# Kernel optimization log

Measured on AMD Instinct MI355X. Metric: run time of the kernel, lower is better.

## Reference

```python
import math
import jax, jax.numpy as jnp
import numpy as np

B, T, C, H = 4, 2048, 1024, 16
D = C // H  # head dim = 64


def setup_inputs() -> dict:
    key = jax.random.key(0)
    ks = jax.random.split(key, 5)
    s = 0.02  # trunc_normal-like init scale
    return {
        "x":  jax.random.normal(ks[0], (B, T, C), dtype=jnp.float32),
        "wq": jax.random.normal(ks[1], (C, C), dtype=jnp.float32) * s,
        "bq": jnp.zeros((C,), dtype=jnp.float32),
        "wk": jax.random.normal(ks[2], (C, C), dtype=jnp.float32) * s,
        "bk": jnp.zeros((C,), dtype=jnp.float32),
        "wv": jax.random.normal(ks[3], (C, C), dtype=jnp.float32) * s,
        "bv": jnp.zeros((C,), dtype=jnp.float32),
        "wp": jax.random.normal(ks[4], (C, C), dtype=jnp.float32) * s,
        "bp": jnp.zeros((C,), dtype=jnp.float32),
    }


def reference(x, wq, bq, wk, bk, wv, bv, wp, bp):
    b, t, c = x.shape
    # QKV projections -> (B, H, T, D)
    q = (x @ wq + bq).reshape(b, t, H, D).transpose(0, 2, 1, 3)
    k = (x @ wk + bk).reshape(b, t, H, D).transpose(0, 2, 1, 3)
    v = (x @ wv + bv).reshape(b, t, H, D).transpose(0, 2, 1, 3)
    present = jnp.stack((k, v))  # (2, B, H, T, D)
    # scaled dot-product with causal mask (layer_past is None path)
    att = jnp.einsum('bhqd,bhkd->bhqk', q, k) * (1.0 / math.sqrt(D))
    causal = jnp.tril(jnp.ones((t, t), dtype=bool))  # (T, T)
    att = jnp.where(causal[None, None], att, -jnp.inf)
    att = jax.nn.softmax(att, axis=-1)
    # dropout prob = 0.0 (eval) -> identity
    y = jnp.einsum('bhqk,bhkd->bhqd', att, v)
    y = y.transpose(0, 2, 1, 3).reshape(b, t, c)
    y = y @ wp + bp
    return (y, present)
```

## Files before the change

kernel.cpp:

```cpp
#include <hip/hip_runtime.h>
#include <hip/hip_bf16.h>
#include <stdint.h>

typedef unsigned short u16;
typedef __bf16 bf16x8 __attribute__((ext_vector_type(8)));
typedef __bf16 bf16x4 __attribute__((ext_vector_type(4)));
typedef float f32x4 __attribute__((ext_vector_type(4)));

#define BB 4
#define TT 2048
#define CC 1024
#define HH 16
#define DD 64

#define QSCALE 0.18033688011112042f

__device__ __forceinline__ u16 f2bf(float f) {
  union { float f; unsigned int u; } v; v.f = f;
  unsigned int u = v.u;
  unsigned int r = (u + 0x7fffu + ((u >> 16) & 1u)) >> 16;
  return (u16)r;
}

__device__ __forceinline__ void async_copy16(const void* g, void* l) {
  __builtin_amdgcn_global_load_lds(
      (const __attribute__((address_space(1))) void*)g,
      (__attribute__((address_space(3))) void*)l, 16, 0, 0);
}

__global__ __launch_bounds__(256) void k_cast_x(const float* __restrict__ x,
                                                u16* __restrict__ xb) {
  int i = (blockIdx.x * 256 + threadIdx.x) * 4;
  float4 f = *reinterpret_cast<const float4*>(x + i);
  ushort4 o;
  o.x = f2bf(f.x); o.y = f2bf(f.y); o.z = f2bf(f.z); o.w = f2bf(f.w);
  *reinterpret_cast<ushort4*>(xb + i) = o;
}

__global__ __launch_bounds__(256) void k_transpose_w(
    const float* __restrict__ w0, const float* __restrict__ w1,
    const float* __restrict__ w2, const float* __restrict__ w3,
    u16* __restrict__ t0, u16* __restrict__ t1,
    u16* __restrict__ t2, u16* __restrict__ t3) {
  const float* w = blockIdx.z == 0 ? w0 : blockIdx.z == 1 ? w1 : blockIdx.z == 2 ? w2 : w3;
  u16* t = blockIdx.z == 0 ? t0 : blockIdx.z == 1 ? t1 : blockIdx.z == 2 ? t2 : t3;
  __shared__ u16 tile[32][33];
  int tx = threadIdx.x, ty = threadIdx.y;
  int k0 = blockIdx.x * 32, n0 = blockIdx.y * 32;
#pragma unroll
  for (int r = 0; r < 4; r++)
    tile[ty + r * 8][tx] = f2bf(w[(size_t)(k0 + ty + r * 8) * CC + n0 + tx]);
  __syncthreads();
#pragma unroll
  for (int r = 0; r < 4; r++)
    t[(size_t)(n0 + ty + r * 8) * CC + k0 + tx] = tile[tx][ty + r * 8];
}

__global__ __launch_bounds__(256) void k_transpose_v(
    const float* __restrict__ out_v, u16* __restrict__ vbt) {
  int tb = blockIdx.x * 64;
  int bh = blockIdx.y;
  const float* src = out_v + (size_t)bh * TT * DD;
  u16* dst = vbt + (size_t)bh * TT * DD;
  __shared__ u16 tile[64][65];
  int tid = threadIdx.x;
#pragma unroll
  for (int p = 0; p < 4; p++) {
    int c = p * 256 + tid;
    int t = c >> 4, d0 = (c & 15) * 4;
    float4 f = *reinterpret_cast<const float4*>(src + (size_t)(tb + t) * DD + d0);
    tile[t][d0 + 0] = f2bf(f.x);
    tile[t][d0 + 1] = f2bf(f.y);
    tile[t][d0 + 2] = f2bf(f.z);
    tile[t][d0 + 3] = f2bf(f.w);
  }
  __syncthreads();
#pragma unroll
  for (int p = 0; p < 2; p++) {
    int c = p * 256 + tid;
    int d = c >> 3, t0 = (c & 7) * 8;
    ushort4 lo, hi;
    lo.x = tile[t0 + 0][d]; lo.y = tile[t0 + 1][d];
    lo.z = tile[t0 + 2][d]; lo.w = tile[t0 + 3][d];
    hi.x = tile[t0 + 4][d]; hi.y = tile[t0 + 5][d];
    hi.z = tile[t0 + 6][d]; hi.w = tile[t0 + 7][d];
    u16* o = dst + (size_t)d * TT + tb + t0;
    *reinterpret_cast<ushort4*>(o) = lo;
    *reinterpret_cast<ushort4*>(o + 4) = hi;
  }
}

#define GEMM_PROLOGUE()                                                        \
  int tid = threadIdx.x;                                                       \
  int lane = tid & 63;                                                         \
  int wave = tid >> 6;                                                         \
  int l15 = lane & 15, quad = lane >> 4;                                       \
  int wave_m = wave & 1, wave_n = wave >> 1;                                   \
  __shared__ u16 lA[128 * 32];                                                 \
  __shared__ u16 lB[128 * 32];                                                 \
  f32x4 acc[4][4] = {};                                                        \
  for (int k0 = 0; k0 < CC; k0 += 32) {                                        \
    __syncthreads();                                                           \
    _Pragma("unroll")                                                          \
    for (int r = 0; r < 2; r++) {                                              \
      int c = r * 256 + tid;                                                   \
      int row = c >> 2, col8 = (c & 3) * 8;                                    \
      async_copy16(A + (size_t)(tile_m + row) * CC + k0 + col8, &lA[c * 8]);   \
    }                                                                          \
    _Pragma("unroll")                                                          \
    for (int r = 0; r < 2; r++) {                                              \
      int c = r * 256 + tid;                                                   \
      int row = c >> 2, col8 = (c & 3) * 8;                                    \
      async_copy16(Bt + (size_t)(tile_n + row) * CC + k0 + col8, &lB[c * 8]);  \
    }                                                                          \
    __syncthreads();                                                           \
    bf16x8 af[4], bfr[4];                                                      \
    _Pragma("unroll")                                                          \
    for (int i = 0; i < 4; i++)                                                \
      af[i] = *reinterpret_cast<const bf16x8*>(                                \
          &lA[(wave_m * 64 + i * 16 + l15) * 32 + quad * 8]);                  \
    _Pragma("unroll")                                                          \
    for (int j = 0; j < 4; j++)                                                \
      bfr[j] = *reinterpret_cast<const bf16x8*>(                               \
          &lB[(wave_n * 64 + j * 16 + l15) * 32 + quad * 8]);                  \
    _Pragma("unroll")                                                          \
    for (int i = 0; i < 4; i++)                                                \
      _Pragma("unroll")                                                        \
      for (int j = 0; j < 4; j++)                                              \
        acc[i][j] =                                                            \
            __builtin_amdgcn_mfma_f32_16x16x32_bf16(af[i], bfr[j], acc[i][j],  \
                                                    0, 0, 0);                  \
  }

__global__ __launch_bounds__(256) void k_gemm_qkv(
    const u16* __restrict__ xb,
    const u16* __restrict__ wtq, const u16* __restrict__ wtk, const u16* __restrict__ wtv,
    const float* __restrict__ bq, const float* __restrict__ bk, const float* __restrict__ bv,
    u16* __restrict__ qb, u16* __restrict__ kb,
    float* __restrict__ out_k, float* __restrict__ out_v) {
  int mat = blockIdx.z;
  const u16* A = xb;
  const u16* Bt = mat == 0 ? wtq : mat == 1 ? wtk : wtv;
  const float* bias = mat == 0 ? bq : mat == 1 ? bk : bv;
  int tile_m = blockIdx.x * 128;
  int tile_n = blockIdx.y * 128;

  GEMM_PROLOGUE()

#pragma unroll
  for (int j = 0; j < 4; j++) {
    int n = tile_n + wave_n * 64 + j * 16 + l15;
    int h = n >> 6, d = n & 63;
    float bias_n = bias[n];
#pragma unroll
    for (int i = 0; i < 4; i++) {
#pragma unroll
      for (int r = 0; r < 4; r++) {
        int m = tile_m + wave_m * 64 + i * 16 + quad * 4 + r;
        int b = m >> 11, t = m & 2047;
        float val = acc[i][j][r] + bias_n;
        size_t idx = (((size_t)(b * HH + h)) * TT + t) * DD + d;
        if (mat == 0) {
          qb[idx] = f2bf(val * QSCALE);
        } else if (mat == 1) {
          out_k[idx] = val;
          kb[idx] = f2bf(val);
        } else {
          out_v[idx] = val;
        }
      }
    }
  }
}

__global__ __launch_bounds__(256) void k_gemm_proj(
    const u16* __restrict__ yb, const u16* __restrict__ wtp,
    const float* __restrict__ bp, float* __restrict__ out) {
  const u16* A = yb;
  const u16* Bt = wtp;
  int tile_m = blockIdx.x * 128;
  int tile_n = blockIdx.y * 128;

  GEMM_PROLOGUE()

#pragma unroll
  for (int j = 0; j < 4; j++) {
    int n = tile_n + wave_n * 64 + j * 16 + l15;
    float bias_n = bp[n];
#pragma unroll
    for (int i = 0; i < 4; i++) {
#pragma unroll
      for (int r = 0; r < 4; r++) {
        int m = tile_m + wave_m * 64 + i * 16 + quad * 4 + r;
        out[(size_t)m * CC + n] = acc[i][j][r] + bias_n;
      }
    }
  }
}

__global__ __launch_bounds__(256) void k_attn(
    const u16* __restrict__ qb, const u16* __restrict__ kbuf,
    const u16* __restrict__ vtb, u16* __restrict__ yatt) {
  int qpair = blockIdx.x;
  int bh = blockIdx.y;
  int tid = threadIdx.x;
  int lane = tid & 63;
  int wave = tid >> 6;
  int l15 = lane & 15, quad = lane >> 4;

  const u16* Q = qb + (size_t)bh * TT * DD;
  const u16* K = kbuf + (size_t)bh * TT * DD;
  const u16* Vt = vtb + (size_t)bh * TT * DD;

  __shared__ u16 kl[2][64 * 64];
  __shared__ u16 vl[2][64 * 64];
  __shared__ u16 pl[4][16 * 64];
  u16* plw = pl[wave];

  int h = bh & 15, b = bh >> 4;

  int c0 = tid, c1 = tid + 256;
  int r0 = c0 >> 3, e0 = (((c0 & 7) * 16) ^ ((r0 & 7) << 4)) >> 1;
  int r1 = c1 >> 3, e1 = (((c1 & 7) * 16) ^ ((r1 & 7) << 4)) >> 1;

  auto stage = [&](int buf, int kb0) {
    async_copy16(K + (size_t)(kb0 + r0) * DD + e0, &kl[buf][c0 * 8]);
    async_copy16(K + (size_t)(kb0 + r1) * DD + e1, &kl[buf][c1 * 8]);
    async_copy16(Vt + (size_t)r0 * TT + kb0 + e0, &vl[buf][c0 * 8]);
    async_copy16(Vt + (size_t)r1 * TT + kb0 + e1, &vl[buf][c1 * 8]);
  };

  u16* prow = plw + l15 * 64;
  int xrp = (l15 & 7) << 4;
  int q8 = quad << 3;

#pragma unroll
  for (int side = 0; side < 2; side++) {
    int qt = side == 0 ? qpair : 31 - qpair;

    int qr = qt * 64 + wave * 16 + l15;
    bf16x8 qf0 = *reinterpret_cast<const bf16x8*>(Q + (size_t)qr * DD + quad * 8);
    bf16x8 qf1 = *reinterpret_cast<const bf16x8*>(Q + (size_t)qr * DD + 32 + quad * 8);

    f32x4 o_acc[4] = {};
    float m_run = -1e30f, l_run = 0.f;

    stage(0, 0);

    for (int kblk = 0; kblk <= qt; kblk++) {
      int cur = kblk & 1;
      if (kblk < qt) {
        stage(cur ^ 1, (kblk + 1) * 64);
        asm volatile("s_waitcnt vmcnt(4)" ::: "memory");
      } else {
        asm volatile("s_waitcnt vmcnt(0)" ::: "memory");
      }
      __builtin_amdgcn_sched_barrier(0);
      __builtin_amdgcn_s_barrier();
      __builtin_amdgcn_sched_barrier(0);

      f32x4 s_acc[4];
      __builtin_amdgcn_s_setprio(1);
#pragma unroll
      for (int nb = 0; nb < 4; nb++) {
        int krow = nb * 16 + l15;
        int xr = (krow & 7) << 4;
        const u16* kp = &kl[cur][krow * 64];
        bf16x8 kf0 = *reinterpret_cast<const bf16x8*>(kp + (((quad * 16) ^ xr) >> 1));
        bf16x8 kf1 = *reinterpret_cast<const bf16x8*>(kp + (((64 + quad * 16) ^ xr) >> 1));
        f32x4 z = {};
        z = __builtin_amdgcn_mfma_f32_16x16x32_bf16(kf0, qf0, z, 0, 0, 0);
        z = __builtin_amdgcn_mfma_f32_16x16x32_bf16(kf1, qf1, z, 0, 0, 0);
        s_acc[nb] = z;
      }
      __builtin_amdgcn_s_setprio(0);

      float mx = -1e30f;
      if (kblk == qt) {
        int qg = wave * 16 + l15;
#pragma unroll
        for (int nb = 0; nb < 4; nb++)
#pragma unroll
          for (int r = 0; r < 4; r++) {
            int kg = nb * 16 + quad * 4 + r;
            float s = s_acc[nb][r];
            s = (kg <= qg) ? s : -1e30f;
            s_acc[nb][r] = s;
            mx = fmaxf(mx, s);
          }
      } else {
#pragma unroll
        for (int nb = 0; nb < 4; nb++)
#pragma unroll
          for (int r = 0; r < 4; r++) mx = fmaxf(mx, s_acc[nb][r]);
      }
      mx = fmaxf(mx, __shfl_xor(mx, 16, 64));
      mx = fmaxf(mx, __shfl_xor(mx, 32, 64));

      if (!__all(mx - m_run <= 8.0f)) {
        float mnew = fmaxf(m_run, mx);
        float alpha = __builtin_amdgcn_exp2f(m_run - mnew);
        m_run = mnew;
        l_run *= alpha;
        float av[4];
#pragma unroll
        for (int r = 0; r < 4; r++) av[r] = __shfl(alpha, quad * 4 + r, 64);
#pragma unroll
        for (int db = 0; db < 4; db++)
#pragma unroll
          for (int r = 0; r < 4; r++) o_acc[db][r] *= av[r];
      }

      float sum = 0.f;
#pragma unroll
      for (int nb = 0; nb < 4; nb++)
#pragma unroll
        for (int r = 0; r < 4; r++) {
          float e = __builtin_amdgcn_exp2f(s_acc[nb][r] - m_run);
          s_acc[nb][r] = e;
          sum += e;
        }
      sum += __shfl_xor(sum, 16, 64);
      sum += __shfl_xor(sum, 32, 64);
      l_run += sum;

#pragma unroll
      for (int nb = 0; nb < 4; nb++) {
        bf16x4 pk = {(__bf16)s_acc[nb][0], (__bf16)s_acc[nb][1],
                     (__bf16)s_acc[nb][2], (__bf16)s_acc[nb][3]};
        *reinterpret_cast<bf16x4*>(prow + ((((nb << 5) + q8) ^ xrp) >> 1)) = pk;
      }

      __builtin_amdgcn_s_setprio(1);
#pragma unroll
      for (int half = 0; half < 2; half++) {
        bf16x8 pf = *reinterpret_cast<const bf16x8*>(
            prow + (((half * 64 + quad * 16) ^ xrp) >> 1));
#pragma unroll
        for (int db = 0; db < 4; db++) {
          int vrow = db * 16 + l15;
          bf16x8 vf = *reinterpret_cast<const bf16x8*>(
              &vl[cur][vrow * 64] + (((half * 64 + quad * 16) ^ ((vrow & 7) << 4)) >> 1));
          o_acc[db] = __builtin_amdgcn_mfma_f32_16x16x32_bf16(pf, vf, o_acc[db], 0, 0, 0);
        }
      }
      __builtin_amdgcn_s_setprio(0);

      __builtin_amdgcn_sched_barrier(0);
      __builtin_amdgcn_s_barrier();
    }

    float lr[4];
#pragma unroll
    for (int r = 0; r < 4; r++) lr[r] = __shfl(l_run, quad * 4 + r, 64);
#pragma unroll
    for (int r = 0; r < 4; r++) {
      float inv = 1.0f / lr[r];
      int tq = qt * 64 + wave * 16 + quad * 4 + r;
#pragma unroll
      for (int db = 0; db < 4; db++) {
        int d = db * 16 + l15;
        yatt[((size_t)(b * TT + tq)) * CC + h * DD + d] = f2bf(o_acc[db][r] * inv);
      }
    }
  }
}

extern "C" void kernel_launch(void* const* d_in, const int* in_sizes, int n_in,
                              void* d_out, int out_size, void* d_ws, size_t ws_size,
                              hipStream_t stream) {
  const float* x  = (const float*)d_in[0];
  const float* wq = (const float*)d_in[1];
  const float* bq = (const float*)d_in[2];
  const float* wk = (const float*)d_in[3];
  const float* bk = (const float*)d_in[4];
  const float* wv = (const float*)d_in[5];
  const float* bv = (const float*)d_in[6];
  const float* wp = (const float*)d_in[7];
  const float* bp = (const float*)d_in[8];

  float* out_y = (float*)d_out;
  float* out_k = out_y + (size_t)BB * TT * CC;
  float* out_v = out_k + (size_t)BB * HH * TT * DD;

  u16* xb  = (u16*)d_ws;
  u16* wtq = xb + (size_t)BB * TT * CC;
  u16* wtk = wtq + (size_t)CC * CC;
  u16* wtv = wtk + (size_t)CC * CC;
  u16* wtp = wtv + (size_t)CC * CC;
  u16* qb  = wtp + (size_t)CC * CC;
  u16* kb  = qb + (size_t)BB * TT * CC;
  u16* vbt = kb + (size_t)BB * TT * CC;
  u16* yb  = vbt + (size_t)BB * TT * CC;

  k_cast_x<<<(BB * TT * CC) / 1024, 256, 0, stream>>>(x, xb);
  k_transpose_w<<<dim3(CC / 32, CC / 32, 4), dim3(32, 8), 0, stream>>>(
      wq, wk, wv, wp, wtq, wtk, wtv, wtp);
  k_gemm_qkv<<<dim3(BB * TT / 128, CC / 128, 3), 256, 0, stream>>>(
      xb, wtq, wtk, wtv, bq, bk, bv, qb, kb, out_k, out_v);
  k_transpose_v<<<dim3(TT / 64, BB * HH), 256, 0, stream>>>(out_v, vbt);
  k_attn<<<dim3(16, BB * HH), 256, 0, stream>>>(qb, kb, vbt, yb);
  k_gemm_proj<<<dim3(BB * TT / 128, CC / 128), 256, 0, stream>>>(yb, wtp, bp, out_y);
}
```

Before: 340.0 us.

## Double-buffer GEMM LDS tiles with async prefetch and XOR swizzle

Converts the shared GEMM main loop to double-buffered LDS, issuing the next k-step's global-to-LDS async copies before computing on the current buffer and waiting only on older loads with explicit vmcnt. Adds an XOR swizzle of the 16-byte column chunks to reduce LDS bank conflicts on fragment reads, and raises wave priority around the MFMA block. The aim is to hide global load latency behind matrix math. It doubles LDS use per block, which may lower occupancy, and relies on hand-placed waitcnt and barriers being correct.

```diff
diff --git a/kernel.cpp b/kernel.cpp
--- a/kernel.cpp
+++ b/kernel.cpp
@@ -96,33 +96,48 @@
   int wave = tid >> 6;                                                         \
   int l15 = lane & 15, quad = lane >> 4;                                       \
   int wave_m = wave & 1, wave_n = wave >> 1;                                   \
-  __shared__ u16 lA[128 * 32];                                                 \
-  __shared__ u16 lB[128 * 32];                                                 \
+  __shared__ u16 lA[2][128 * 32];                                              \
+  __shared__ u16 lB[2][128 * 32];                                              \
   f32x4 acc[4][4] = {};                                                        \
-  for (int k0 = 0; k0 < CC; k0 += 32) {                                        \
-    __syncthreads();                                                           \
+  int s_c0 = tid, s_c1 = tid + 256;                                            \
+  int s_r0 = s_c0 >> 2, s_e0 = ((s_c0 & 3) ^ ((s_c0 >> 3) & 3)) * 8;           \
+  int s_r1 = s_c1 >> 2, s_e1 = ((s_c1 & 3) ^ ((s_c1 >> 3) & 3)) * 8;           \
+  auto gstage = [&](int buf, int k0) {                                         \
+    async_copy16(A + (size_t)(tile_m + s_r0) * CC + k0 + s_e0,                 \
+                 &lA[buf][s_c0 * 8]);                                          \
+    async_copy16(A + (size_t)(tile_m + s_r1) * CC + k0 + s_e1,                 \
+                 &lA[buf][s_c1 * 8]);                                          \
+    async_copy16(Bt + (size_t)(tile_n + s_r0) * CC + k0 + s_e0,                \
+                 &lB[buf][s_c0 * 8]);                                          \
+    async_copy16(Bt + (size_t)(tile_n + s_r1) * CC + k0 + s_e1,                \
+                 &lB[buf][s_c1 * 8]);                                          \
+  };                                                                           \
+  gstage(0, 0);                                                                \
+  for (int ks = 0; ks < CC / 32; ks++) {                                       \
+    int curb = ks & 1;                                                         \
+    if (ks < CC / 32 - 1) {                                                    \
+      gstage(curb ^ 1, (ks + 1) * 32);                                         \
+      asm volatile("s_waitcnt vmcnt(4)" ::: "memory");                         \
+    } else {                                                                   \
+      asm volatile("s_waitcnt vmcnt(0)" ::: "memory");                         \
+    }                                                                          \
+    __builtin_amdgcn_sched_barrier(0);                                         \
+    __builtin_amdgcn_s_barrier();                                              \
+    __builtin_amdgcn_sched_barrier(0);                                         \
+    bf16x8 af[4], bfr[4];                                                      \
     _Pragma("unroll")                                                          \
-    for (int r = 0; r < 2; r++) {                                              \
-      int c = r * 256 + tid;                                                   \
-      int row = c >> 2, col8 = (c & 3) * 8;                                    \
-      async_copy16(A + (size_t)(tile_m + row) * CC + k0 + col8, &lA[c * 8]);   \
+    for (int i = 0; i < 4; i++) {                                              \
+      int rA = wave_m * 64 + i * 16 + l15;                                     \
+      int qs = quad ^ ((rA >> 1) & 3);                                         \
+      af[i] = *reinterpret_cast<const bf16x8*>(&lA[curb][rA * 32 + qs * 8]);   \
     }                                                                          \
     _Pragma("unroll")                                                          \
-    for (int r = 0; r < 2; r++) {                                              \
-      int c = r * 256 + tid;                                                   \
-      int row = c >> 2, col8 = (c & 3) * 8;                                    \
-      async_copy16(Bt + (size_t)(tile_n + row) * CC + k0 + col8, &lB[c * 8]);  \
+    for (int j = 0; j < 4; j++) {                                              \
+      int rB = wave_n * 64 + j * 16 + l15;                                     \
+      int qs = quad ^ ((rB >> 1) & 3);                                         \
+      bfr[j] = *reinterpret_cast<const bf16x8*>(&lB[curb][rB * 32 + qs * 8]);  \
     }                                                                          \
-    __syncthreads();                                                           \
-    bf16x8 af[4], bfr[4];                                                      \
-    _Pragma("unroll")                                                          \
-    for (int i = 0; i < 4; i++)                                                \
-      af[i] = *reinterpret_cast<const bf16x8*>(                                \
-          &lA[(wave_m * 64 + i * 16 + l15) * 32 + quad * 8]);                  \
-    _Pragma("unroll")                                                          \
-    for (int j = 0; j < 4; j++)                                                \
-      bfr[j] = *reinterpret_cast<const bf16x8*>(                               \
-          &lB[(wave_n * 64 + j * 16 + l15) * 32 + quad * 8]);                  \
+    __builtin_amdgcn_s_setprio(1);                                             \
     _Pragma("unroll")                                                          \
     for (int i = 0; i < 4; i++)                                                \
       _Pragma("unroll")                                                        \
@@ -130,6 +145,9 @@
         acc[i][j] =                                                            \
             __builtin_amdgcn_mfma_f32_16x16x32_bf16(af[i], bfr[j], acc[i][j],  \
                                                     0, 0, 0);                  \
+    __builtin_amdgcn_s_setprio(0);                                             \
+    __builtin_amdgcn_sched_barrier(0);                                         \
+    __builtin_amdgcn_s_barrier();                                              \
   }
 
 __global__ __launch_bounds__(256) void k_gemm_qkv(
```

New measurement: 346.1 us. No clear change (+1.8%).

## Triple-buffer GEMM with async prefetch, XOR-swizzled LDS, and 256x128 tiles

Applied to the files above, without the earlier changes.

Rewrites the shared GEMM mainloop used by the QKV and output projections. It now uses 512-thread blocks with 256x128 tiles and BK=64, keeps three LDS buffers so global loads for k+2 overlap compute on k, and waits on vmcnt instead of doing two block barriers per step. LDS rows are XOR-swizzled to avoid bank conflicts on the MFMA fragment reads, and s_setprio is raised around the MFMA block. The cost is about 144KB of LDS per block and half as many blocks, which limits occupancy to one block per CU.

```diff
diff --git a/kernel.cpp b/kernel.cpp
--- a/kernel.cpp
+++ b/kernel.cpp
@@ -95,44 +95,85 @@
   int lane = tid & 63;                                                         \
   int wave = tid >> 6;                                                         \
   int l15 = lane & 15, quad = lane >> 4;                                       \
-  int wave_m = wave & 1, wave_n = wave >> 1;                                   \
-  __shared__ u16 lA[128 * 32];                                                 \
-  __shared__ u16 lB[128 * 32];                                                 \
+  int wr = wave >> 1, wc = wave & 1;                                           \
+  __shared__ u16 lA[3][256 * 64];                                              \
+  __shared__ u16 lB[3][128 * 64];                                              \
   f32x4 acc[4][4] = {};                                                        \
-  for (int k0 = 0; k0 < CC; k0 += 32) {                                        \
-    __syncthreads();                                                           \
-    _Pragma("unroll")                                                          \
-    for (int r = 0; r < 2; r++) {                                              \
-      int c = r * 256 + tid;                                                   \
-      int row = c >> 2, col8 = (c & 3) * 8;                                    \
-      async_copy16(A + (size_t)(tile_m + row) * CC + k0 + col8, &lA[c * 8]);   \
-    }                                                                          \
-    _Pragma("unroll")                                                          \
-    for (int r = 0; r < 2; r++) {                                              \
-      int c = r * 256 + tid;                                                   \
-      int row = c >> 2, col8 = (c & 3) * 8;                                    \
-      async_copy16(Bt + (size_t)(tile_n + row) * CC + k0 + col8, &lB[c * 8]);  \
-    }                                                                          \
-    __syncthreads();                                                           \
-    bf16x8 af[4], bfr[4];                                                      \
+  int arow[4], aoff[4];                                                        \
+  _Pragma("unroll")                                                            \
+  for (int i = 0; i < 4; i++) {                                                \
+    int c = tid + i * 512;                                                     \
+    arow[i] = c >> 3;                                                          \
+    aoff[i] = (((c & 7) * 16) ^ ((arow[i] & 7) << 4)) >> 1;                    \
+  }                                                                            \
+  int brow[2], boff[2];                                                        \
+  _Pragma("unroll")                                                            \
+  for (int i = 0; i < 2; i++) {                                                \
+    int c = tid + i * 512;                                                     \
+    brow[i] = c >> 3;                                                          \
+    boff[i] = (((c & 7) * 16) ^ ((brow[i] & 7) << 4)) >> 1;                    \
+  }                                                                            \
+  auto gstage = [&](int buf, int k0) {                                         \
     _Pragma("unroll")                                                          \
     for (int i = 0; i < 4; i++)                                                \
-      af[i] = *reinterpret_cast<const bf16x8*>(                                \
-          &lA[(wave_m * 64 + i * 16 + l15) * 32 + quad * 8]);                  \
+      async_copy16(A + (size_t)(tile_m + arow[i]) * CC + k0 + aoff[i],         \
+                   &lA[buf][(tid + i * 512) * 8]);                             \
     _Pragma("unroll")                                                          \
-    for (int j = 0; j < 4; j++)                                                \
-      bfr[j] = *reinterpret_cast<const bf16x8*>(                               \
-          &lB[(wave_n * 64 + j * 16 + l15) * 32 + quad * 8]);                  \
+    for (int i = 0; i < 2; i++)                                                \
+      async_copy16(Bt + (size_t)(tile_n + brow[i]) * CC + k0 + boff[i],        \
+                   &lB[buf][(tid + i * 512) * 8]);                             \
+  };                                                                           \
+  int offA[4][2], offB[4][2];                                                  \
+  _Pragma("unroll")                                                            \
+  for (int i = 0; i < 4; i++) {                                                \
+    int rA = wr * 64 + i * 16 + l15;                                           \
+    int xrA = (rA & 7) << 4;                                                   \
+    offA[i][0] = rA * 64 + (((quad * 16) ^ xrA) >> 1);                         \
+    offA[i][1] = rA * 64 + (((64 + quad * 16) ^ xrA) >> 1);                    \
+    int rB = wc * 64 + i * 16 + l15;                                           \
+    int xrB = (rB & 7) << 4;                                                   \
+    offB[i][0] = rB * 64 + (((quad * 16) ^ xrB) >> 1);                         \
+    offB[i][1] = rB * 64 + (((64 + quad * 16) ^ xrB) >> 1);                    \
+  }                                                                            \
+  gstage(0, 0);                                                                \
+  gstage(1, 64);                                                               \
+  int rcur = 0, rstage = 2;                                                    \
+  for (int kt = 0; kt < 16; kt++) {                                            \
+    if (kt < 15)                                                               \
+      asm volatile("s_waitcnt vmcnt(6)" ::: "memory");                         \
+    else                                                                       \
+      asm volatile("s_waitcnt vmcnt(0)" ::: "memory");                         \
+    __builtin_amdgcn_sched_barrier(0);                                         \
+    __builtin_amdgcn_s_barrier();                                              \
+    __builtin_amdgcn_sched_barrier(0);                                         \
+    if (kt + 2 < 16) gstage(rstage, (kt + 2) * 64);                            \
+    bf16x8 af[4][2], bfv[4][2];                                                \
+    _Pragma("unroll")                                                          \
+    for (int i = 0; i < 4; i++) {                                              \
+      af[i][0] = *reinterpret_cast<const bf16x8*>(&lA[rcur][offA[i][0]]);      \
+      af[i][1] = *reinterpret_cast<const bf16x8*>(&lA[rcur][offA[i][1]]);      \
+      bfv[i][0] = *reinterpret_cast<const bf16x8*>(&lB[rcur][offB[i][0]]);     \
+      bfv[i][1] = *reinterpret_cast<const bf16x8*>(&lB[rcur][offB[i][1]]);     \
+    }                                                                          \
+    __builtin_amdgcn_s_setprio(1);                                             \
     _Pragma("unroll")                                                          \
     for (int i = 0; i < 4; i++)                                                \
       _Pragma("unroll")                                                        \
       for (int j = 0; j < 4; j++)                                              \
-        acc[i][j] =                                                            \
-            __builtin_amdgcn_mfma_f32_16x16x32_bf16(af[i], bfr[j], acc[i][j],  \
-                                                    0, 0, 0);                  \
-  }
-
-__global__ __launch_bounds__(256) void k_gemm_qkv(
+        acc[i][j] = __builtin_amdgcn_mfma_f32_16x16x32_bf16(                   \
+            af[i][0], bfv[j][0], acc[i][j], 0, 0, 0);                          \
+    _Pragma("unroll")                                                          \
+    for (int i = 0; i < 4; i++)                                                \
+      _Pragma("unroll")                                                        \
+      for (int j = 0; j < 4; j++)                                              \
+        acc[i][j] = __builtin_amdgcn_mfma_f32_16x16x32_bf16(                   \
+            af[i][1], bfv[j][1], acc[i][j], 0, 0, 0);                          \
+    __builtin_amdgcn_s_setprio(0);                                             \
+    rcur = (rcur == 2) ? 0 : rcur + 1;                                         \
+    rstage = (rstage == 2) ? 0 : rstage + 1;                                   \
+  }
+
+__global__ __launch_bounds__(512) void k_gemm_qkv(
     const u16* __restrict__ xb,
     const u16* __restrict__ wtq, const u16* __restrict__ wtk, const u16* __restrict__ wtv,
     const float* __restrict__ bq, const float* __restrict__ bk, const float* __restrict__ bv,
@@ -142,21 +183,21 @@
   const u16* A = xb;
   const u16* Bt = mat == 0 ? wtq : mat == 1 ? wtk : wtv;
   const float* bias = mat == 0 ? bq : mat == 1 ? bk : bv;
-  int tile_m = blockIdx.x * 128;
+  int tile_m = blockIdx.x * 256;
   int tile_n = blockIdx.y * 128;
 
   GEMM_PROLOGUE()
 
 #pragma unroll
   for (int j = 0; j < 4; j++) {
-    int n = tile_n + wave_n * 64 + j * 16 + l15;
+    int n = tile_n + wc * 64 + j * 16 + l15;
     int h = n >> 6, d = n & 63;
     float bias_n = bias[n];
 #pragma unroll
     for (int i = 0; i < 4; i++) {
 #pragma unroll
       for (int r = 0; r < 4; r++) {
-        int m = tile_m + wave_m * 64 + i * 16 + quad * 4 + r;
+        int m = tile_m + wr * 64 + i * 16 + quad * 4 + r;
         int b = m >> 11, t = m & 2047;
         float val = acc[i][j][r] + bias_n;
         size_t idx = (((size_t)(b * HH + h)) * TT + t) * DD + d;
@@ -173,25 +214,25 @@
   }
 }
 
-__global__ __launch_bounds__(256) void k_gemm_proj(
+__global__ __launch_bounds__(512) void k_gemm_proj(
     const u16* __restrict__ yb, const u16* __restrict__ wtp,
     const float* __restrict__ bp, float* __restrict__ out) {
   const u16* A = yb;
   const u16* Bt = wtp;
-  int tile_m = blockIdx.x * 128;
+  int tile_m = blockIdx.x * 256;
   int tile_n = blockIdx.y * 128;
 
   GEMM_PROLOGUE()
 
 #pragma unroll
   for (int j = 0; j < 4; j++) {
-    int n = tile_n + wave_n * 64 + j * 16 + l15;
+    int n = tile_n + wc * 64 + j * 16 + l15;
     float bias_n = bp[n];
 #pragma unroll
     for (int i = 0; i < 4; i++) {
 #pragma unroll
       for (int r = 0; r < 4; r++) {
-        int m = tile_m + wave_m * 64 + i * 16 + quad * 4 + r;
+        int m = tile_m + wr * 64 + i * 16 + quad * 4 + r;
         out[(size_t)m * CC + n] = acc[i][j][r] + bias_n;
       }
     }
@@ -396,9 +437,9 @@
   k_cast_x<<<(BB * TT * CC) / 1024, 256, 0, stream>>>(x, xb);
   k_transpose_w<<<dim3(CC / 32, CC / 32, 4), dim3(32, 8), 0, stream>>>(
       wq, wk, wv, wp, wtq, wtk, wtv, wtp);
-  k_gemm_qkv<<<dim3(BB * TT / 128, CC / 128, 3), 256, 0, stream>>>(
+  k_gemm_qkv<<<dim3(BB * TT / 256, CC / 128, 3), 512, 0, stream>>>(
       xb, wtq, wtk, wtv, bq, bk, bv, qb, kb, out_k, out_v);
   k_transpose_v<<<dim3(TT / 64, BB * HH), 256, 0, stream>>>(out_v, vbt);
   k_attn<<<dim3(16, BB * HH), 256, 0, stream>>>(qb, kb, vbt, yb);
-  k_gemm_proj<<<dim3(BB * TT / 128, CC / 128), 256, 0, stream>>>(yb, wtp, bp, out_y);
-}
+  k_gemm_proj<<<dim3(BB * TT / 256, CC / 128), 512, 0, stream>>>(yb, wtp, bp, out_y);
+}
```

Result: no change. 345.7 us (+1.7%).

## Rewrite projection GEMMs as 256x256 double-buffered pipelined tiles and fuse prep kernels

Applied to the files above, without the earlier changes.

Replaces the 128x128 single-buffered GEMM loop with 256x256 tiles over 8 waves. The new loop double-buffers 64-wide k slices in LDS, interleaves async loads with MFMA phases, swizzles LDS addresses to avoid bank conflicts, and raises wave priority around MFMA. It also merges the x cast and weight transposes into one launch. The intent is to raise reuse per byte loaded and hide global latency, at the cost of large LDS use and fewer blocks, which leaves the projection GEMM with fewer blocks than CUs.

```diff
diff --git a/kernel.cpp b/kernel.cpp
--- a/kernel.cpp
+++ b/kernel.cpp
@@ -28,32 +28,35 @@
       (__attribute__((address_space(3))) void*)l, 16, 0, 0);
 }
 
-__global__ __launch_bounds__(256) void k_cast_x(const float* __restrict__ x,
-                                                u16* __restrict__ xb) {
-  int i = (blockIdx.x * 256 + threadIdx.x) * 4;
-  float4 f = *reinterpret_cast<const float4*>(x + i);
-  ushort4 o;
-  o.x = f2bf(f.x); o.y = f2bf(f.y); o.z = f2bf(f.z); o.w = f2bf(f.w);
-  *reinterpret_cast<ushort4*>(xb + i) = o;
-}
-
-__global__ __launch_bounds__(256) void k_transpose_w(
+__global__ __launch_bounds__(256) void k_prep(
+    const float* __restrict__ x, u16* __restrict__ xb,
     const float* __restrict__ w0, const float* __restrict__ w1,
     const float* __restrict__ w2, const float* __restrict__ w3,
     u16* __restrict__ t0, u16* __restrict__ t1,
     u16* __restrict__ t2, u16* __restrict__ t3) {
-  const float* w = blockIdx.z == 0 ? w0 : blockIdx.z == 1 ? w1 : blockIdx.z == 2 ? w2 : w3;
-  u16* t = blockIdx.z == 0 ? t0 : blockIdx.z == 1 ? t1 : blockIdx.z == 2 ? t2 : t3;
-  __shared__ u16 tile[32][33];
+  int z = blockIdx.z;
   int tx = threadIdx.x, ty = threadIdx.y;
-  int k0 = blockIdx.x * 32, n0 = blockIdx.y * 32;
-#pragma unroll
-  for (int r = 0; r < 4; r++)
-    tile[ty + r * 8][tx] = f2bf(w[(size_t)(k0 + ty + r * 8) * CC + n0 + tx]);
-  __syncthreads();
-#pragma unroll
-  for (int r = 0; r < 4; r++)
-    t[(size_t)(n0 + ty + r * 8) * CC + k0 + tx] = tile[tx][ty + r * 8];
+  if (z < 4) {
+    const float* w = z == 0 ? w0 : z == 1 ? w1 : z == 2 ? w2 : w3;
+    u16* t = z == 0 ? t0 : z == 1 ? t1 : z == 2 ? t2 : t3;
+    __shared__ u16 tile[32][33];
+    int k0 = blockIdx.x * 32, n0 = blockIdx.y * 32;
+#pragma unroll
+    for (int r = 0; r < 4; r++)
+      tile[ty + r * 8][tx] = f2bf(w[(size_t)(k0 + ty + r * 8) * CC + n0 + tx]);
+    __syncthreads();
+#pragma unroll
+    for (int r = 0; r < 4; r++)
+      t[(size_t)(n0 + ty + r * 8) * CC + k0 + tx] = tile[tx][ty + r * 8];
+  } else {
+    int bid = (z - 4) * 1024 + blockIdx.y * 32 + blockIdx.x;
+    int tid = ty * 32 + tx;
+    int i = (bid * 256 + tid) * 4;
+    float4 f = *reinterpret_cast<const float4*>(x + i);
+    ushort4 o;
+    o.x = f2bf(f.x); o.y = f2bf(f.y); o.z = f2bf(f.z); o.w = f2bf(f.w);
+    *reinterpret_cast<ushort4*>(xb + i) = o;
+  }
 }
 
 __global__ __launch_bounds__(256) void k_transpose_v(
@@ -90,49 +93,121 @@
   }
 }
 
-#define GEMM_PROLOGUE()                                                        \
+#define MFMA16(AF, BF, ACCBASE)                                                \
+  _Pragma("unroll")                                                            \
+  for (int i = 0; i < 4; i++)                                                  \
+    _Pragma("unroll")                                                          \
+    for (int j = 0; j < 4; j++)                                                \
+      acc[(ACCBASE) + i][j] = __builtin_amdgcn_mfma_f32_16x16x32_bf16(         \
+          AF[i], BF[j], acc[(ACCBASE) + i][j], 0, 0, 0);
+
+#define GEMM8_PROLOGUE()                                                       \
   int tid = threadIdx.x;                                                       \
   int lane = tid & 63;                                                         \
   int wave = tid >> 6;                                                         \
   int l15 = lane & 15, quad = lane >> 4;                                       \
-  int wave_m = wave & 1, wave_n = wave >> 1;                                   \
-  __shared__ u16 lA[128 * 32];                                                 \
-  __shared__ u16 lB[128 * 32];                                                 \
-  f32x4 acc[4][4] = {};                                                        \
-  for (int k0 = 0; k0 < CC; k0 += 32) {                                        \
-    __syncthreads();                                                           \
-    _Pragma("unroll")                                                          \
-    for (int r = 0; r < 2; r++) {                                              \
-      int c = r * 256 + tid;                                                   \
-      int row = c >> 2, col8 = (c & 3) * 8;                                    \
-      async_copy16(A + (size_t)(tile_m + row) * CC + k0 + col8, &lA[c * 8]);   \
-    }                                                                          \
-    _Pragma("unroll")                                                          \
-    for (int r = 0; r < 2; r++) {                                              \
-      int c = r * 256 + tid;                                                   \
-      int row = c >> 2, col8 = (c & 3) * 8;                                    \
-      async_copy16(Bt + (size_t)(tile_n + row) * CC + k0 + col8, &lB[c * 8]);  \
-    }                                                                          \
-    __syncthreads();                                                           \
-    bf16x8 af[4], bfr[4];                                                      \
+  int wr = wave >> 2, wc = wave & 3;                                           \
+  __shared__ u16 sA[2][2][256 * 32];                                           \
+  __shared__ u16 sB[2][2][256 * 32];                                           \
+  f32x4 acc[8][4] = {};                                                        \
+  int g_r0 = tid >> 2, g_e0 = ((tid & 3) ^ ((tid >> 3) & 3)) * 8;              \
+  int g_c1 = tid + 512;                                                        \
+  int g_r1 = g_c1 >> 2, g_e1 = ((g_c1 & 3) ^ ((g_c1 >> 3) & 3)) * 8;           \
+  auto stageA = [&](int d, int kh, int k0) {                                   \
+    async_copy16(A + (size_t)(tile_m + g_r0) * CC + k0 + kh * 32 + g_e0,       \
+                 &sA[d][kh][tid * 8]);                                         \
+    async_copy16(A + (size_t)(tile_m + g_r1) * CC + k0 + kh * 32 + g_e1,       \
+                 &sA[d][kh][g_c1 * 8]);                                        \
+  };                                                                           \
+  auto stageB = [&](int d, int kh, int k0) {                                   \
+    async_copy16(Bt + (size_t)(tile_n + g_r0) * CC + k0 + kh * 32 + g_e0,      \
+                 &sB[d][kh][tid * 8]);                                         \
+    async_copy16(Bt + (size_t)(tile_n + g_r1) * CC + k0 + kh * 32 + g_e1,      \
+                 &sB[d][kh][g_c1 * 8]);                                        \
+  };                                                                           \
+  int offA[8], offB[4];                                                        \
+  _Pragma("unroll")                                                            \
+  for (int mi = 0; mi < 8; mi++) {                                             \
+    int RA = wr * 128 + mi * 16 + l15;                                         \
+    offA[mi] = RA * 32 + (quad ^ ((RA >> 1) & 3)) * 8;                         \
+  }                                                                            \
+  _Pragma("unroll")                                                            \
+  for (int j = 0; j < 4; j++) {                                                \
+    int RB = wc * 64 + j * 16 + l15;                                           \
+    offB[j] = RB * 32 + (quad ^ ((RB >> 1) & 3)) * 8;                          \
+  }                                                                            \
+  stageA(0, 0, 0); stageB(0, 0, 0); stageA(0, 1, 0); stageB(0, 1, 0);          \
+  for (int kt = 0; kt < 16; kt++) {                                            \
+    int d = kt & 1;                                                            \
+    int kn = (kt + 1) * 64;                                                    \
+                                        \
+    asm volatile("s_waitcnt vmcnt(4)" ::: "memory");                           \
+    __builtin_amdgcn_sched_barrier(0);                                         \
+    __builtin_amdgcn_s_barrier();                                              \
+    __builtin_amdgcn_sched_barrier(0);                                         \
+    if (kt < 15) stageA(d ^ 1, 0, kn);                                         \
+    bf16x8 b0[4], af[4];                                                       \
+    _Pragma("unroll")                                                          \
+    for (int j = 0; j < 4; j++)                                                \
+      b0[j] = *reinterpret_cast<const bf16x8*>(&sB[d][0][offB[j]]);            \
     _Pragma("unroll")                                                          \
     for (int i = 0; i < 4; i++)                                                \
-      af[i] = *reinterpret_cast<const bf16x8*>(                                \
-          &lA[(wave_m * 64 + i * 16 + l15) * 32 + quad * 8]);                  \
+      af[i] = *reinterpret_cast<const bf16x8*>(&sA[d][0][offA[i]]);            \
+    asm volatile("s_waitcnt lgkmcnt(0)" ::: "memory");                         \
+    __builtin_amdgcn_sched_barrier(0);                                         \
+    __builtin_amdgcn_s_setprio(1);                                             \
+    MFMA16(af, b0, 0)                                                          \
+    __builtin_amdgcn_s_setprio(0);                                             \
+                                        \
+    __builtin_amdgcn_sched_barrier(0);                                         \
+    __builtin_amdgcn_s_barrier();                                              \
+    __builtin_amdgcn_sched_barrier(0);                                         \
+    if (kt < 15) stageB(d ^ 1, 0, kn);                                         \
+    _Pragma("unroll")                                                          \
+    for (int i = 0; i < 4; i++)                                                \
+      af[i] = *reinterpret_cast<const bf16x8*>(&sA[d][0][offA[4 + i]]);        \
+    asm volatile("s_waitcnt lgkmcnt(0)" ::: "memory");                         \
+    __builtin_amdgcn_sched_barrier(0);                                         \
+    __builtin_amdgcn_s_setprio(1);                                             \
+    MFMA16(af, b0, 4)                                                          \
+    __builtin_amdgcn_s_setprio(0);                                             \
+                                        \
+    if (kt < 15)                                                               \
+      asm volatile("s_waitcnt vmcnt(4)" ::: "memory");                         \
+    else                                                                       \
+      asm volatile("s_waitcnt vmcnt(0)" ::: "memory");                         \
+    __builtin_amdgcn_sched_barrier(0);                                         \
+    __builtin_amdgcn_s_barrier();                                              \
+    __builtin_amdgcn_sched_barrier(0);                                         \
+    if (kt < 15) stageA(d ^ 1, 1, kn);                                         \
+    bf16x8 b1[4];                                                              \
     _Pragma("unroll")                                                          \
     for (int j = 0; j < 4; j++)                                                \
-      bfr[j] = *reinterpret_cast<const bf16x8*>(                               \
-          &lB[(wave_n * 64 + j * 16 + l15) * 32 + quad * 8]);                  \
+      b1[j] = *reinterpret_cast<const bf16x8*>(&sB[d][1][offB[j]]);            \
     _Pragma("unroll")                                                          \
     for (int i = 0; i < 4; i++)                                                \
-      _Pragma("unroll")                                                        \
-      for (int j = 0; j < 4; j++)                                              \
-        acc[i][j] =                                                            \
-            __builtin_amdgcn_mfma_f32_16x16x32_bf16(af[i], bfr[j], acc[i][j],  \
-                                                    0, 0, 0);                  \
-  }
-
-__global__ __launch_bounds__(256) void k_gemm_qkv(
+      af[i] = *reinterpret_cast<const bf16x8*>(&sA[d][1][offA[i]]);            \
+    asm volatile("s_waitcnt lgkmcnt(0)" ::: "memory");                         \
+    __builtin_amdgcn_sched_barrier(0);                                         \
+    __builtin_amdgcn_s_setprio(1);                                             \
+    MFMA16(af, b1, 0)                                                          \
+    __builtin_amdgcn_s_setprio(0);                                             \
+                                        \
+    __builtin_amdgcn_sched_barrier(0);                                         \
+    __builtin_amdgcn_s_barrier();                                              \
+    __builtin_amdgcn_sched_barrier(0);                                         \
+    if (kt < 15) stageB(d ^ 1, 1, kn);                                         \
+    _Pragma("unroll")                                                          \
+    for (int i = 0; i < 4; i++)                                                \
+      af[i] = *reinterpret_cast<const bf16x8*>(&sA[d][1][offA[4 + i]]);        \
+    asm volatile("s_waitcnt lgkmcnt(0)" ::: "memory");                         \
+    __builtin_amdgcn_sched_barrier(0);                                         \
+    __builtin_amdgcn_s_setprio(1);                                             \
+    MFMA16(af, b1, 4)                                                          \
+    __builtin_amdgcn_s_setprio(0);                                             \
+  }
+
+__global__ __launch_bounds__(512, 2) void k_gemm_qkv(
     const u16* __restrict__ xb,
     const u16* __restrict__ wtq, const u16* __restrict__ wtk, const u16* __restrict__ wtv,
     const float* __restrict__ bq, const float* __restrict__ bk, const float* __restrict__ bv,
@@ -142,24 +217,24 @@
   const u16* A = xb;
   const u16* Bt = mat == 0 ? wtq : mat == 1 ? wtk : wtv;
   const float* bias = mat == 0 ? bq : mat == 1 ? bk : bv;
-  int tile_m = blockIdx.x * 128;
-  int tile_n = blockIdx.y * 128;
-
-  GEMM_PROLOGUE()
+  int tile_m = blockIdx.x * 256;
+  int tile_n = blockIdx.y * 256;
+
+  GEMM8_PROLOGUE()
 
 #pragma unroll
   for (int j = 0; j < 4; j++) {
-    int n = tile_n + wave_n * 64 + j * 16 + l15;
-    int h = n >> 6, d = n & 63;
+    int n = tile_n + wc * 64 + j * 16 + l15;
+    int h = n >> 6, dd = n & 63;
     float bias_n = bias[n];
 #pragma unroll
-    for (int i = 0; i < 4; i++) {
+    for (int mi = 0; mi < 8; mi++) {
 #pragma unroll
       for (int r = 0; r < 4; r++) {
-        int m = tile_m + wave_m * 64 + i * 16 + quad * 4 + r;
+        int m = tile_m + wr * 128 + mi * 16 + quad * 4 + r;
         int b = m >> 11, t = m & 2047;
-        float val = acc[i][j][r] + bias_n;
-        size_t idx = (((size_t)(b * HH + h)) * TT + t) * DD + d;
+        float val = acc[mi][j][r] + bias_n;
+        size_t idx = (((size_t)(b * HH + h)) * TT + t) * DD + dd;
         if (mat == 0) {
           qb[idx] = f2bf(val * QSCALE);
         } else if (mat == 1) {
@@ -173,26 +248,26 @@
   }
 }
 
-__global__ __launch_bounds__(256) void k_gemm_proj(
+__global__ __launch_bounds__(512, 2) void k_gemm_proj(
     const u16* __restrict__ yb, const u16* __restrict__ wtp,
     const float* __restrict__ bp, float* __restrict__ out) {
   const u16* A = yb;
   const u16* Bt = wtp;
-  int tile_m = blockIdx.x * 128;
-  int tile_n = blockIdx.y * 128;
-
-  GEMM_PROLOGUE()
+  int tile_m = blockIdx.x * 256;
+  int tile_n = blockIdx.y * 256;
+
+  GEMM8_PROLOGUE()
 
 #pragma unroll
   for (int j = 0; j < 4; j++) {
-    int n = tile_n + wave_n * 64 + j * 16 + l15;
+    int n = tile_n + wc * 64 + j * 16 + l15;
     float bias_n = bp[n];
 #pragma unroll
-    for (int i = 0; i < 4; i++) {
+    for (int mi = 0; mi < 8; mi++) {
 #pragma unroll
       for (int r = 0; r < 4; r++) {
-        int m = tile_m + wave_m * 64 + i * 16 + quad * 4 + r;
-        out[(size_t)m * CC + n] = acc[i][j][r] + bias_n;
+        int m = tile_m + wr * 128 + mi * 16 + quad * 4 + r;
+        out[(size_t)m * CC + n] = acc[mi][j][r] + bias_n;
       }
     }
   }
@@ -393,12 +468,11 @@
   u16* vbt = kb + (size_t)BB * TT * CC;
   u16* yb  = vbt + (size_t)BB * TT * CC;
 
-  k_cast_x<<<(BB * TT * CC) / 1024, 256, 0, stream>>>(x, xb);
-  k_transpose_w<<<dim3(CC / 32, CC / 32, 4), dim3(32, 8), 0, stream>>>(
-      wq, wk, wv, wp, wtq, wtk, wtv, wtp);
-  k_gemm_qkv<<<dim3(BB * TT / 128, CC / 128, 3), 256, 0, stream>>>(
+  k_prep<<<dim3(32, 32, 12), dim3(32, 8), 0, stream>>>(
+      x, xb, wq, wk, wv, wp, wtq, wtk, wtv, wtp);
+  k_gemm_qkv<<<dim3(BB * TT / 256, CC / 256, 3), 512, 0, stream>>>(
       xb, wtq, wtk, wtv, bq, bk, bv, qb, kb, out_k, out_v);
   k_transpose_v<<<dim3(TT / 64, BB * HH), 256, 0, stream>>>(out_v, vbt);
   k_attn<<<dim3(16, BB * HH), 256, 0, stream>>>(qb, kb, vbt, yb);
-  k_gemm_proj<<<dim3(BB * TT / 128, CC / 128), 256, 0, stream>>>(yb, wtp, bp, out_y);
-}
+  k_gemm_proj<<<dim3(BB * TT / 256, CC / 256), 512, 0, stream>>>(yb, wtp, bp, out_y);
+}
```

Measured after the change: 358.7 us. +5.5%, slower.
